# Performance work log

Measured on AMD Instinct MI355X. Metric: run time of the kernel, lower is better.

Reference implementation:

```python
import jax, jax.numpy as jnp
import numpy as np

B, S, D, H = 4, 2048, 1024, 16
HD = D // H
ROPE_THETA = 10000.0


def setup_inputs() -> dict:
    key = jax.random.key(0)
    ks = jax.random.split(key, 5)
    scale = 1.0 / np.sqrt(D)
    inp = {
        "x": jax.random.normal(ks[0], (B, S, D), dtype=jnp.float32),
        "Wq": jax.random.normal(ks[1], (D, D), dtype=jnp.float32) * scale,
        "bq": jnp.zeros((D,), jnp.float32),
        "Wk": jax.random.normal(ks[2], (D, D), dtype=jnp.float32) * scale,
        "bk": jnp.zeros((D,), jnp.float32),
        "Wv": jax.random.normal(ks[3], (D, D), dtype=jnp.float32) * scale,
        "bv": jnp.zeros((D,), jnp.float32),
        "Wo": jax.random.normal(ks[4], (D, D), dtype=jnp.float32) * scale,
        "bo": jnp.zeros((D,), jnp.float32),
        # causal mask: True means masked (j > i), matching masked_fill semantics
        "attn_mask": jnp.triu(jnp.ones((S, S), dtype=bool), k=1),
    }
    return inp


def _rope(x):
    # x: [B, H, S, HD]; half-split rotary embedding
    half = HD // 2
    inv_freq = 1.0 / (ROPE_THETA ** (jnp.arange(0, half, dtype=jnp.float32) / half))
    pos = jnp.arange(x.shape[2], dtype=jnp.float32)
    freqs = pos[:, None] * inv_freq[None, :]            # [S, half]
    cos = jnp.cos(freqs)[None, None]                    # [1,1,S,half]
    sin = jnp.sin(freqs)[None, None]
    x1, x2 = x[..., :half], x[..., half:]
    return jnp.concatenate([x1 * cos - x2 * sin, x2 * cos + x1 * sin], axis=-1)


def reference(x, Wq, bq, Wk, bk, Wv, bv, Wo, bo, attn_mask):
    def shape(t):  # [B,S,D] -> [B,H,S,HD]
        return t.reshape(B, S, H, HD).transpose(0, 2, 1, 3)

    q = shape(x @ Wq.T + bq)
    k = shape(x @ Wk.T + bk)
    v = shape(x @ Wv.T + bv)
    q = _rope(q)
    k = _rope(k)
    scores = jnp.einsum("bhqd,bhkd->bhqk", q, k) * (HD ** -0.5)
    scores = jnp.where(attn_mask[None, None], -jnp.inf, scores)
    w = jax.nn.softmax(scores, axis=-1)
    attn = jnp.einsum("bhqk,bhkd->bhqd", w, v)
    merged = attn.transpose(0, 2, 1, 3).reshape(B, S, D)
    return merged @ Wo.T + bo
```

## Files before the change

### kernel.cpp

```cpp
#include <hip/hip_runtime.h>
#include <math.h>

#define BATCH 4
#define SEQ   2048
#define DMODEL 1024
#define NHEAD 16
#define HDIM  64
#define MROWS (BATCH*SEQ)

typedef unsigned short u16;
typedef unsigned int   u32;

using bf16x8 = __attribute__((ext_vector_type(8))) short;
using f32x4  = __attribute__((ext_vector_type(4))) float;
using f32x16 = __attribute__((ext_vector_type(16))) float;
using u32x4  = __attribute__((ext_vector_type(4))) unsigned int;

__device__ __forceinline__ u16 f2bf(float f) {
    u32 u = __float_as_uint(f);
    u += 0x7fffu + ((u >> 16) & 1u);
    return (u16)(u >> 16);
}
__device__ __forceinline__ u32 pack2bf(float a, float b) {
    u32 ua = __float_as_uint(a); ua += 0x7fffu + ((ua >> 16) & 1u);
    u32 ub = __float_as_uint(b); ub += 0x7fffu + ((ub >> 16) & 1u);
    return (ua >> 16) | (ub & 0xffff0000u);
}
__device__ __forceinline__ u32 cvtpk(float a, float b) {
    u32 r;
    asm("v_cvt_pk_bf16_f32 %0, %1, %2" : "=v"(r) : "v"(a), "v"(b));
    return r;
}
#define PLSWAP(a, b) asm("v_permlane32_swap_b32 %0, %1" : "+v"(a), "+v"(b))

#define GLOBAL_LOAD_LDS16(gp, lp)                                              \
    __builtin_amdgcn_global_load_lds(                                          \
        (const __attribute__((address_space(1))) void*)(gp),                   \
        (__attribute__((address_space(3))) void*)(lp), 16, 0, 0)

__global__ __launch_bounds__(256) void convert_inputs(
    const float* __restrict__ x,  const float* __restrict__ wq,
    const float* __restrict__ wk, const float* __restrict__ wv,
    const float* __restrict__ wo, u16* __restrict__ dst)
{
    long long i4 = ((long long)blockIdx.x * 256 + threadIdx.x) * 4;
    const float* src; long long off;
    if (i4 < 8388608LL) { src = x; off = i4; }
    else {
        long long j = i4 - 8388608LL;
        int seg = (int)(j >> 20);
        off = j & 1048575LL;
        src = (seg == 0) ? wq : (seg == 1) ? wk : (seg == 2) ? wv : wo;
    }
    float4 v = *(const float4*)(src + off);
    u32 lo = (u32)f2bf(v.x) | ((u32)f2bf(v.y) << 16);
    u32 hi = (u32)f2bf(v.z) | ((u32)f2bf(v.w) << 16);
    *(uint2*)(dst + i4) = make_uint2(lo, hi);
}

template<int EPI>
__global__ __launch_bounds__(512) void gemm8(
    const u16* __restrict__ A, const u16* __restrict__ W,
    const float* __restrict__ b0_, const float* __restrict__ b1_,
    u16* __restrict__ C0_, u16* __restrict__ C1_, float* __restrict__ Cf)
{
    __shared__ __align__(16) u16 smem[65536];

    const int t    = threadIdx.x;
    const int lane = t & 63;
    const int w    = t >> 6;
    const int quad = lane >> 4;
    const int l15  = lane & 15;
    const int wm   = w >> 2;
    const int wn   = w & 3;

    const int bx  = blockIdx.x;
    const int xcd = bx & 7;
    const int i_  = bx >> 3;
    const int bml = i_ & 3;
    const int n_  = i_ >> 2;

    const int bm = (xcd * 4 + bml) * 256;
    const int bn = n_ * 256;

    const bool   isq  = (bn < 1024);
    const float* bias = isq ? b0_ : b1_;
    u16*         Cb   = isq ? C0_ : C1_;
    const int    bnl  = bn & 1023;

    const int sr8 = lane >> 3;
    const int scl = (lane & 7) ^ sr8;
    const u16* gA = A + (size_t)(bm + 8 * w + sr8) * DMODEL + scl * 8;
    const u16* gB = W + (size_t)(bn + 8 * w + sr8) * DMODEL + scl * 8;

#define STG_A(rg, kt, bs)                                                      \
    GLOBAL_LOAD_LDS16(gA + (size_t)(rg) * 64 * DMODEL + (kt) * 64,             \
                      &smem[(bs) * 16384 + ((rg) * 64 + 8 * w) * 64])
#define STG_B(rg, kt, bs)                                                      \
    GLOBAL_LOAD_LDS16(gB + (size_t)(rg) * 64 * DMODEL + (kt) * 64,             \
                      &smem[32768 + (bs) * 16384 + ((rg) * 64 + 8 * w) * 64])

    STG_B(0, 0, 0); STG_B(1, 0, 0); STG_B(2, 0, 0); STG_B(3, 0, 0);
    STG_A(0, 0, 0); STG_A(2, 0, 0); STG_A(1, 0, 0); STG_A(3, 0, 0);
    STG_B(0, 1, 1); STG_B(1, 1, 1); STG_B(2, 1, 1); STG_B(3, 1, 1);
    STG_A(0, 1, 1); STG_A(2, 1, 1);
    asm volatile("s_waitcnt vmcnt(6)" ::: "memory");
    __builtin_amdgcn_s_barrier();

    const int cA0 = (quad ^ (l15 & 7)) * 8;

    f32x4 acc[8][4] = {};
    bf16x8 bfr[4][2];

#define LOAD_B(Bb) {                                                           \
    _Pragma("unroll")                                                          \
    for (int j = 0; j < 4; ++j) {                                              \
        bfr[j][0] = *(const bf16x8*)&(Bb)[(wn * 64 + 16 * j + l15) * 64 + cA0];\
        bfr[j][1] = *(const bf16x8*)&(Bb)[(wn * 64 + 16 * j + l15) * 64 + (cA0 ^ 32)];\
    } }
#define PHASE(q, Ab, Bb, STAGES, CKPT) {                                       \
    bf16x8 af_[2][2];                                                          \
    if ((q) == 0) LOAD_B(Bb);                                                  \
    _Pragma("unroll")                                                          \
    for (int ii = 0; ii < 2; ++ii) {                                           \
        const int r_ = (wm * 128 + (q) * 32 + 16 * ii + l15) * 64;             \
        af_[ii][0] = *(const bf16x8*)&(Ab)[r_ + cA0];                          \
        af_[ii][1] = *(const bf16x8*)&(Ab)[r_ + (cA0 ^ 32)];                   \
    }                                                                          \
    STAGES;                                                                    \
    __builtin_amdgcn_s_barrier();                                              \
    asm volatile("s_waitcnt lgkmcnt(0)" ::: "memory");                         \
    __builtin_amdgcn_sched_barrier(0);                                         \
    __builtin_amdgcn_s_setprio(1);                                             \
    _Pragma("unroll")                                                          \
    for (int ii = 0; ii < 2; ++ii)                                             \
        _Pragma("unroll")                                                      \
        for (int j = 0; j < 4; ++j) {                                          \
            acc[2*(q)+ii][j] = __builtin_amdgcn_mfma_f32_16x16x32_bf16(        \
                af_[ii][0], bfr[j][0], acc[2*(q)+ii][j], 0, 0, 0);             \
            acc[2*(q)+ii][j] = __builtin_amdgcn_mfma_f32_16x16x32_bf16(        \
                af_[ii][1], bfr[j][1], acc[2*(q)+ii][j], 0, 0, 0);             \
        }                                                                      \
    __builtin_amdgcn_s_setprio(0);                                             \
    CKPT;                                                                      \
    __builtin_amdgcn_s_barrier();                                              \
}

    #pragma unroll 1
    for (int i = 0; i < 8; ++i) {
        const bool st = (i < 7);
        const int  kn = 2 * i + 2, kn3 = 2 * i + 3, ko = 2 * i + 1;
        {
            const u16* Ab = smem;
            const u16* Bb = smem + 32768;
            PHASE(0, Ab, Bb, { STG_A(1, ko, 1); STG_A(3, ko, 1); }, {});
            PHASE(1, Ab, Bb, { if (st) { STG_B(0, kn, 0); STG_B(1, kn, 0); } }, {});
            PHASE(2, Ab, Bb, { if (st) { STG_B(2, kn, 0); STG_B(3, kn, 0); } }, {});
            PHASE(3, Ab, Bb, { if (st) { STG_A(0, kn, 0); STG_A(2, kn, 0); } },
                  { if (st) asm volatile("s_waitcnt vmcnt(6)" ::: "memory");
                    else    asm volatile("s_waitcnt vmcnt(0)" ::: "memory"); });
        }
        {
            const u16* Ab = smem + 16384;
            const u16* Bb = smem + 32768 + 16384;
            PHASE(0, Ab, Bb, { if (st) { STG_A(1, kn, 0); STG_A(3, kn, 0); } }, {});
            PHASE(1, Ab, Bb, { if (st) { STG_B(0, kn3, 1); STG_B(1, kn3, 1); } }, {});
            PHASE(2, Ab, Bb, { if (st) { STG_B(2, kn3, 1); STG_B(3, kn3, 1); } }, {});
            PHASE(3, Ab, Bb, { if (st) { STG_A(0, kn3, 1); STG_A(2, kn3, 1); } },
                  { if (st) asm volatile("s_waitcnt vmcnt(6)" ::: "memory");
                    else    asm volatile("s_waitcnt vmcnt(0)" ::: "memory"); });
        }
    }
#undef PHASE
#undef LOAD_B
#undef STG_A
#undef STG_B

    const int wrow = wm * 128;
    const int wcol = wn * 64;
    float bvv[4];
    #pragma unroll
    for (int j = 0; j < 4; j++) bvv[j] = bias[bnl + wcol + 16 * j + l15];

    const float qscale = isq ? 0.18033688011112042f : 1.0f;
    float inv[2];
    #pragma unroll
    for (int j = 0; j < 2; j++) {
        int d = 16 * j + l15;
        inv[j] = exp2f(-(float)d * 0.4152410118609203f);
    }
    #pragma unroll
    for (int ri = 0; ri < 8; ri++)
        #pragma unroll
        for (int r = 0; r < 4; r++) {
            int mg = bm + wrow + 16 * ri + quad * 4 + r;
            int s  = mg & (SEQ - 1);
            #pragma unroll
            for (int j = 0; j < 2; j++) {
                float f = (float)s * inv[j];
                float sn, cs;
                __sincosf(f, &sn, &cs);
                float a1 = acc[ri][j][r]     + bvv[j];
                float a2 = acc[ri][j + 2][r] + bvv[j + 2];
                float o1 = (a1 * cs - a2 * sn) * qscale;
                float o2 = (a2 * cs + a1 * sn) * qscale;
                Cb[(size_t)mg * DMODEL + bnl + wcol + 16 * j       + l15] = f2bf(o1);
                Cb[(size_t)mg * DMODEL + bnl + wcol + 16 * (j + 2) + l15] = f2bf(o2);
            }
        }
}

template<int MODE>
__global__ __launch_bounds__(512) void gemm_bn128(
    const u16* __restrict__ A, const u16* __restrict__ W,
    const float* __restrict__ bias_, u16* __restrict__ Cb, float* __restrict__ Cf)
{
    __shared__ u16 As[3 * 256 * 64];
    __shared__ u16 Ws[3 * 128 * 64];

    const int t    = threadIdx.x;
    const int lane = t & 63;
    const int w    = t >> 6;
    const int quad = lane >> 4;
    const int l15  = lane & 15;

    const int bx  = blockIdx.x;
    const int xcd = bx & 7;
    const int i_  = bx >> 3;
    const int bml = i_ & 3;
    const int n_  = i_ >> 2;

    const int bm   = (xcd * 4 + bml) * 256;
    const int bn   = n_ * 128;
    const int wrow = (w >> 1) * 64;
    const int wcol = (w & 1) * 64;

    const int sr8 = lane >> 3;
    const int scl = (lane & 7) ^ sr8;
    const u16* gA = A + (size_t)(bm + 8 * w + sr8) * DMODEL + scl * 8;
    const u16* gB = W + (size_t)(bn + 8 * w + sr8) * DMODEL + scl * 8;

#define STAGE_A(li, kt, bs)                                                    \
    GLOBAL_LOAD_LDS16(gA + (size_t)(li) * 64 * DMODEL + (kt) * 64,             \
                      &As[(bs) * 16384 + ((li) * 64 + 8 * w) * 64])
#define STAGE_B(li, kt, bs)                                                    \
    GLOBAL_LOAD_LDS16(gB + (size_t)(li) * 64 * DMODEL + (kt) * 64,             \
                      &Ws[(bs) * 8192 + ((li) * 64 + 8 * w) * 64])

    STAGE_A(0, 0, 0); STAGE_A(1, 0, 0); STAGE_A(2, 0, 0); STAGE_A(3, 0, 0);
    STAGE_B(0, 0, 0); STAGE_B(1, 0, 0);
    STAGE_A(0, 1, 1); STAGE_A(1, 1, 1); STAGE_A(2, 1, 1); STAGE_A(3, 1, 1);
    STAGE_B(0, 1, 1); STAGE_B(1, 1, 1);
    asm volatile("s_waitcnt vmcnt(6)" ::: "memory");
    __builtin_amdgcn_s_barrier();

    const int c0 = (quad ^ (l15 & 7)) * 8;
    const int c1 = c0 ^ 32;

    f32x4 acc[4][4] = {};

    int bsel = 0;
    #pragma unroll 1
    for (int kt = 0; kt < DMODEL / 64; ++kt) {
        const u16* Ab = &As[bsel * 16384];
        const u16* Bb = &Ws[bsel * 8192];
        const int  ks = kt + 2;
        const int  sb = (bsel >= 1) ? bsel - 1 : 2;
        const bool st = (ks < DMODEL / 64);

        bf16x8 af[4], bfr[4];

        #pragma unroll
        for (int i = 0; i < 4; ++i)
            af[i] = *(const bf16x8*)&Ab[(wrow + 16 * i + l15) * 64 + c0];
        #pragma unroll
        for (int j = 0; j < 4; ++j)
            bfr[j] = *(const bf16x8*)&Bb[(wcol + 16 * j + l15) * 64 + c0];
        if (st) { STAGE_A(0, ks, sb); STAGE_A(1, ks, sb); STAGE_A(2, ks, sb); }
        __builtin_amdgcn_s_barrier();
        __builtin_amdgcn_s_setprio(1);
        #pragma unroll
        for (int i = 0; i < 4; ++i)
            #pragma unroll
            for (int j = 0; j < 4; ++j)
                acc[i][j] = __builtin_amdgcn_mfma_f32_16x16x32_bf16(af[i], bfr[j], acc[i][j], 0, 0, 0);
        __builtin_amdgcn_s_setprio(0);
        __builtin_amdgcn_s_barrier();

        #pragma unroll
        for (int i = 0; i < 4; ++i)
            af[i] = *(const bf16x8*)&Ab[(wrow + 16 * i + l15) * 64 + c1];
        #pragma unroll
        for (int j = 0; j < 4; ++j)
            bfr[j] = *(const bf16x8*)&Bb[(wcol + 16 * j + l15) * 64 + c1];
        if (st) { STAGE_A(3, ks, sb); STAGE_B(0, ks, sb); STAGE_B(1, ks, sb); }
        __builtin_amdgcn_s_barrier();
        __builtin_amdgcn_s_setprio(1);
        #pragma unroll
        for (int i = 0; i < 4; ++i)
            #pragma unroll
            for (int j = 0; j < 4; ++j)
                acc[i][j] = __builtin_amdgcn_mfma_f32_16x16x32_bf16(af[i], bfr[j], acc[i][j], 0, 0, 0);
        __builtin_amdgcn_s_setprio(0);
        if (st) asm volatile("s_waitcnt vmcnt(6)" ::: "memory");
        else    asm volatile("s_waitcnt vmcnt(0)" ::: "memory");
        __builtin_amdgcn_s_barrier();

        bsel = (bsel == 2) ? 0 : bsel + 1;
    }
#undef STAGE_A
#undef STAGE_B

    float bv[4];
    #pragma unroll
    for (int j = 0; j < 4; j++) bv[j] = bias_[bn + wcol + 16 * j + l15];

    if constexpr (MODE == 0) {
        #pragma unroll
        for (int i = 0; i < 4; i++)
            #pragma unroll
            for (int r = 0; r < 4; r++) {
                int mg = bm + wrow + 16 * i + quad * 4 + r;
                #pragma unroll
                for (int j = 0; j < 4; j++)
                    Cf[(size_t)mg * DMODEL + bn + wcol + 16 * j + l15] = acc[i][j][r] + bv[j];
            }
    } else {
        u16* T = As;
        #pragma unroll
        for (int i = 0; i < 4; i++) {
            #pragma unroll
            for (int j = 0; j < 4; j++) {
                int col = wrow + 16 * i + quad * 4;
                int row = wcol + 16 * j + l15;
                u32 lo = pack2bf(acc[i][j][0] + bv[j], acc[i][j][1] + bv[j]);
                u32 hi = pack2bf(acc[i][j][2] + bv[j], acc[i][j][3] + bv[j]);
                *(uint2*)((char*)T + row * 512 + ((col * 2) ^ ((row & 3) << 4)))
                    = make_uint2(lo, hi);
            }
        }
        __syncthreads();
        {
            int row  = t >> 2, colc = t & 3;
            int hgl  = (bn + row) >> 6;
            int dl   = (bn + row) & 63;
            int bb   = bm >> 11;
            size_t obase = (((size_t)(bb * NHEAD + hgl)) * HDIM + dl) * SEQ
                         + (bm & (SEQ - 1)) + colc * 64;
            #pragma unroll
            for (int k = 0; k < 8; k++) {
                uint4 vv = *(const uint4*)((const char*)T + row * 512
                             + ((colc * 128 + k * 16) ^ ((row & 3) << 4)));
                *(uint4*)(Cb + obase + k * 8) = vv;
            }
        }
    }
}

__global__ __launch_bounds__(256) void attn_mfma(
    const u16* __restrict__ Q, const u16* __restrict__ K,
    const u16* __restrict__ VT, u16* __restrict__ O)
{
    __shared__ __align__(16) u16 smem[16640];
    u16* const Qs  = smem;
    u16* const Ks0 = smem + 8192;
    u16* const Ks1 = smem;
    u16* const Vt0 = smem + 12288;
    u16* const Vt1 = smem + 4096;
    float* const lS = (float*)(smem + 16384);

    const int t    = threadIdx.x;
    const int lane = t & 63;
    const int w    = t >> 6;
    const int l31  = lane & 31;
    const int hl   = lane >> 5;
    const int bid  = blockIdx.x;
    const int bh   = bid & 63;
    const int x_   = bid >> 6, g_ = x_ >> 2, r_ = x_ & 3;
    const int qt   = (g_ == 0) ? 15 - r_ : (g_ == 1) ? 8 + r_
                   : (g_ == 2) ? 4 + r_ : 3 - r_;
    const int h    = bh & (NHEAD - 1);
    const int b    = bh >> 4;
    const int q0   = qt * 128;

    const size_t gbase = ((size_t)b * SEQ) * DMODEL + h * HDIM;
    const size_t vbase = ((size_t)(b * NHEAD + h)) * HDIM * SEQ;

    const int rl  = lane >> 3;
    const int csw = (lane & 7) ^ rl;

    #pragma unroll
    for (int i = 0; i < 4; i++) {
        int row = 32 * w + 8 * i + rl;
        GLOBAL_LOAD_LDS16(Q + gbase + (size_t)(q0 + row) * DMODEL + csw * 8,
                          &Qs[(32 * w + 8 * i) * 64]);
    }
    #pragma unroll
    for (int i = 0; i < 2; i++) {
        int row = 16 * w + 8 * i + rl;
        GLOBAL_LOAD_LDS16(K + gbase + (size_t)row * DMODEL + csw * 8,
                          &Ks0[(16 * w + 8 * i) * 64]);
        GLOBAL_LOAD_LDS16(VT + vbase + (size_t)row * SEQ + csw * 8,
                          &Vt0[(16 * w + 8 * i) * 64]);
    }
    __syncthreads();

    bf16x8 qf[4];
    {
        int row = 32 * w + l31;
        #pragma unroll
        for (int s = 0; s < 4; s++) {
            int c = (hl + 2 * s) ^ (row & 7);
            qf[s] = *(const bf16x8*)&Qs[row * 64 + c * 8];
        }
    }
    __syncthreads();

    float lsum = 0.0f;
    f32x16 oacc[2] = {};
    const int qg   = q0 + 32 * w + l31;
    const int qmax = q0 + 32 * w + 31;

#define QUADRANT(KRH, F0, F1) do {                                             \
    f32x16 s_ = {};                                                            \
    __builtin_amdgcn_s_setprio(1);                                             \
    _Pragma("unroll")                                                          \
    for (int stp_ = 0; stp_ < 4; ++stp_) {                                     \
        int c_ = ((hl + 2 * stp_) ^ (l31 & 7)) * 8;                            \
        bf16x8 ka_ = *(const bf16x8*)&Ksb[(32 * (KRH) + l31) * 64 + c_];       \
        s_ = __builtin_amdgcn_mfma_f32_32x32x16_bf16(ka_, qf[stp_], s_, 0, 0, 0);\
    }                                                                          \
    __builtin_amdgcn_s_setprio(0);                                             \
    if (k0 + 32 * (KRH) + 31 > q0 + 32 * w) {                                  \
        _Pragma("unroll")                                                      \
        for (int rr_ = 0; rr_ < 16; ++rr_) {                                   \
            int krg_ = k0 + 32 * (KRH) + (rr_ & 3) + 8 * (rr_ >> 2) + 4 * hl;  \
            if (krg_ > qg) s_[rr_] = -1e30f;                                   \
        }                                                                      \
    }                                                                          \
    float pv_[16];                                                             \
    _Pragma("unroll")                                                          \
    for (int rr_ = 0; rr_ < 16; ++rr_) pv_[rr_] = __builtin_amdgcn_exp2f(s_[rr_]);\
    lsum += ((pv_[0]+pv_[1])+(pv_[2]+pv_[3])) + ((pv_[4]+pv_[5])+(pv_[6]+pv_[7]))\
          + ((pv_[8]+pv_[9])+(pv_[10]+pv_[11])) + ((pv_[12]+pv_[13])+(pv_[14]+pv_[15]));\
    u32 k01_ = cvtpk(pv_[0], pv_[1]),   k23_ = cvtpk(pv_[2], pv_[3]);          \
    u32 k45_ = cvtpk(pv_[4], pv_[5]),   k67_ = cvtpk(pv_[6], pv_[7]);          \
    u32 k89_ = cvtpk(pv_[8], pv_[9]),   kab_ = cvtpk(pv_[10], pv_[11]);        \
    u32 kcd_ = cvtpk(pv_[12], pv_[13]), kef_ = cvtpk(pv_[14], pv_[15]);        \
    PLSWAP(k01_, k45_); PLSWAP(k23_, k67_);                                    \
    PLSWAP(k89_, kcd_); PLSWAP(kab_, kef_);                                    \
    { union { u32x4 u; bf16x8 v; } c0_; c0_.u = (u32x4){k01_, k23_, k45_, k67_};\
      F0 = c0_.v; }                                                            \
    { union { u32x4 u; bf16x8 v; } c1_; c1_.u = (u32x4){k89_, kab_, kcd_, kef_};\
      F1 = c1_.v; }                                                            \
} while (0)

#define PVSTEP(STP, PF) do {                                                   \
    int c_ = ((hl + 2 * (STP)) ^ (l31 & 7)) * 8;                               \
    bf16x8 v0_ = *(const bf16x8*)&Vtb[l31 * 64 + c_];                          \
    bf16x8 v1_ = *(const bf16x8*)&Vtb[(32 + l31) * 64 + c_];                   \
    oacc[0] = __builtin_amdgcn_mfma_f32_32x32x16_bf16(PF, v0_, oacc[0], 0, 0, 0);\
    oacc[1] = __builtin_amdgcn_mfma_f32_32x32x16_bf16(PF, v1_, oacc[1], 0, 0, 0);\
} while (0)

    const int ktn = 2 * qt + 2;
    for (int kt = 0; kt < ktn; kt++) {
        const int k0 = kt * 64;
        u16* const Ksb = (kt & 1) ? Ks1 : Ks0;
        u16* const Vtb = (kt & 1) ? Vt1 : Vt0;

        if (kt + 1 < ktn) {
            u16* const Ksn = (kt & 1) ? Ks0 : Ks1;
            u16* const Vtn = (kt & 1) ? Vt0 : Vt1;
            const size_t kk0 = (size_t)(kt + 1) * 64;
            #pragma unroll
            for (int i = 0; i < 2; i++) {
                int row = 16 * w + 8 * i + rl;
                GLOBAL_LOAD_LDS16(K + gbase + (kk0 + row) * DMODEL + csw * 8,
                                  &Ksn[(16 * w + 8 * i) * 64]);
                GLOBAL_LOAD_LDS16(VT + vbase + (size_t)row * SEQ + kk0 + csw * 8,
                                  &Vtn[(16 * w + 8 * i) * 64]);
            }
        }

        if (k0 <= qmax) {
            const bool q2 = (k0 + 32 <= qmax);
            bf16x8 pa0, pa1, pa2, pa3;
            QUADRANT(0, pa0, pa1);
            __builtin_amdgcn_s_setprio(1);
            PVSTEP(0, pa0); PVSTEP(1, pa1);
            __builtin_amdgcn_s_setprio(0);
            if (q2) {
                QUADRANT(1, pa2, pa3);
                __builtin_amdgcn_s_setprio(1);
                PVSTEP(2, pa2); PVSTEP(3, pa3);
                __builtin_amdgcn_s_setprio(0);
            }
        }
        asm volatile("s_waitcnt vmcnt(0)" ::: "memory");
        __builtin_amdgcn_s_barrier();
    }
#undef QUADRANT
#undef PVSTEP

    lsum += __shfl_xor(lsum, 32, 64);
    if (lane < 32) lS[32 * w + lane] = lsum;
    __syncthreads();

    #pragma unroll
    for (int g = 0; g < 4; g++) {
        f32x4 lv = *(const f32x4*)&lS[32 * w + 8 * g + 4 * hl];
        #pragma unroll
        for (int rr = 0; rr < 4; rr++) {
            int qg2 = q0 + 32 * w + rr + 8 * g + 4 * hl;
            float inv = 1.0f / lv[rr];
            #pragma unroll
            for (int dh = 0; dh < 2; dh++) {
                float o = oacc[dh][4 * g + rr] * inv;
                O[gbase + (size_t)qg2 * DMODEL + 32 * dh + l31] = f2bf(o);
            }
        }
    }
}

extern "C" void kernel_launch(void* const* d_in, const int* in_sizes, int n_in,
                              void* d_out, int out_size, void* d_ws, size_t ws_size,
                              hipStream_t stream)
{
    const float* x  = (const float*)d_in[0];
    const float* Wq = (const float*)d_in[1];
    const float* bq = (const float*)d_in[2];
    const float* Wk = (const float*)d_in[3];
    const float* bk = (const float*)d_in[4];
    const float* Wv = (const float*)d_in[5];
    const float* bv = (const float*)d_in[6];
    const float* Wo = (const float*)d_in[7];
    const float* bo = (const float*)d_in[8];

    u16* wsp = (u16*)d_ws;
    u16* xb  = wsp;
    u16* Wqb = wsp + 8388608;
    u16* Wkb = Wqb + 1048576;
    u16* Wvb = Wkb + 1048576;
    u16* Wob = Wvb + 1048576;
    u16* Qb  = Wob + 1048576;
    u16* Kb  = Qb + 8388608;
    u16* Vb  = Kb + 8388608;
    u16* Ab  = Vb + 8388608;

    convert_inputs<<<12288, 256, 0, stream>>>(x, Wq, Wk, Wv, Wo, xb);

    gemm8<0><<<256, 512, 0, stream>>>(xb, Wqb, bq, bk, Qb, Kb, nullptr);

    gemm_bn128<1><<<256, 512, 0, stream>>>(xb, Wvb, bv, Vb, nullptr);

    attn_mfma<<<1024, 256, 0, stream>>>(Qb, Kb, Vb, Ab);

    gemm_bn128<0><<<256, 512, 0, stream>>>(Ab, Wob, bo, nullptr, (float*)d_out);
}
```

Before: 256.1 us.

## Compute softmax row sums via MFMA with ones and change LDS swizzle

Replaces the per-thread VALU summation of exponentiated scores with an extra MFMA per PV step that multiplies the bf16 probabilities by a ones vector, so the row sums land in the same accumulator layout as the output. This removes the shuffle, the LDS staging of sums and a block barrier in the epilogue. It also changes the XOR swizzle of Q/K/V tiles in LDS to also depend on row>>3, aiming to cut bank conflicts. The cost is one extra MFMA per PV step (a third more PV matrix work), and the sums are now taken over bf16-rounded probabilities, which slightly changes numerics.

```diff
diff --git a/kernel.cpp b/kernel.cpp
--- a/kernel.cpp
+++ b/kernel.cpp
@@ -361,13 +361,12 @@
     const u16* __restrict__ Q, const u16* __restrict__ K,
     const u16* __restrict__ VT, u16* __restrict__ O)
 {
-    __shared__ __align__(16) u16 smem[16640];
+    __shared__ __align__(16) u16 smem[16384];
     u16* const Qs  = smem;
     u16* const Ks0 = smem + 8192;
     u16* const Ks1 = smem;
     u16* const Vt0 = smem + 12288;
     u16* const Vt1 = smem + 4096;
-    float* const lS = (float*)(smem + 16384);
 
     const int t    = threadIdx.x;
     const int lane = t & 63;
@@ -387,20 +386,22 @@
     const size_t vbase = ((size_t)(b * NHEAD + h)) * HDIM * SEQ;
 
     const int rl  = lane >> 3;
-    const int csw = (lane & 7) ^ rl;
+    const int cs0 = (lane & 7) ^ rl;
 
     #pragma unroll
     for (int i = 0; i < 4; i++) {
         int row = 32 * w + 8 * i + rl;
-        GLOBAL_LOAD_LDS16(Q + gbase + (size_t)(q0 + row) * DMODEL + csw * 8,
+        int c   = cs0 ^ i;
+        GLOBAL_LOAD_LDS16(Q + gbase + (size_t)(q0 + row) * DMODEL + c * 8,
                           &Qs[(32 * w + 8 * i) * 64]);
     }
     #pragma unroll
     for (int i = 0; i < 2; i++) {
         int row = 16 * w + 8 * i + rl;
-        GLOBAL_LOAD_LDS16(K + gbase + (size_t)row * DMODEL + csw * 8,
+        int c   = cs0 ^ ((2 * w + i) & 3);
+        GLOBAL_LOAD_LDS16(K + gbase + (size_t)row * DMODEL + c * 8,
                           &Ks0[(16 * w + 8 * i) * 64]);
-        GLOBAL_LOAD_LDS16(VT + vbase + (size_t)row * SEQ + csw * 8,
+        GLOBAL_LOAD_LDS16(VT + vbase + (size_t)row * SEQ + c * 8,
                           &Vt0[(16 * w + 8 * i) * 64]);
     }
     __syncthreads();
@@ -408,25 +409,31 @@
     bf16x8 qf[4];
     {
         int row = 32 * w + l31;
+        int rk  = (l31 & 7) ^ (l31 >> 3);
         #pragma unroll
         for (int s = 0; s < 4; s++) {
-            int c = (hl + 2 * s) ^ (row & 7);
+            int c = (hl + 2 * s) ^ rk;
             qf[s] = *(const bf16x8*)&Qs[row * 64 + c * 8];
         }
     }
     __syncthreads();
 
-    float lsum = 0.0f;
+    bf16x8 onesf;
+    #pragma unroll
+    for (int e = 0; e < 8; e++) onesf[e] = (short)0x3F80;
+
     f32x16 oacc[2] = {};
+    f32x16 lacc    = {};
     const int qg   = q0 + 32 * w + l31;
     const int qmax = q0 + 32 * w + 31;
+    const int rk31 = (l31 & 7) ^ (l31 >> 3);
 
 #define QUADRANT(KRH, F0, F1) do {                                             \
     f32x16 s_ = {};                                                            \
     __builtin_amdgcn_s_setprio(1);                                             \
     _Pragma("unroll")                                                          \
     for (int stp_ = 0; stp_ < 4; ++stp_) {                                     \
-        int c_ = ((hl + 2 * stp_) ^ (l31 & 7)) * 8;                            \
+        int c_ = ((hl + 2 * stp_) ^ rk31) * 8;                                 \
         bf16x8 ka_ = *(const bf16x8*)&Ksb[(32 * (KRH) + l31) * 64 + c_];       \
         s_ = __builtin_amdgcn_mfma_f32_32x32x16_bf16(ka_, qf[stp_], s_, 0, 0, 0);\
     }                                                                          \
@@ -441,8 +448,6 @@
     float pv_[16];                                                             \
     _Pragma("unroll")                                                          \
     for (int rr_ = 0; rr_ < 16; ++rr_) pv_[rr_] = __builtin_amdgcn_exp2f(s_[rr_]);\
-    lsum += ((pv_[0]+pv_[1])+(pv_[2]+pv_[3])) + ((pv_[4]+pv_[5])+(pv_[6]+pv_[7]))\
-          + ((pv_[8]+pv_[9])+(pv_[10]+pv_[11])) + ((pv_[12]+pv_[13])+(pv_[14]+pv_[15]));\
     u32 k01_ = cvtpk(pv_[0], pv_[1]),   k23_ = cvtpk(pv_[2], pv_[3]);          \
     u32 k45_ = cvtpk(pv_[4], pv_[5]),   k67_ = cvtpk(pv_[6], pv_[7]);          \
     u32 k89_ = cvtpk(pv_[8], pv_[9]),   kab_ = cvtpk(pv_[10], pv_[11]);        \
@@ -456,11 +461,12 @@
 } while (0)
 
 #define PVSTEP(STP, PF) do {                                                   \
-    int c_ = ((hl + 2 * (STP)) ^ (l31 & 7)) * 8;                               \
+    int c_ = ((hl + 2 * (STP)) ^ rk31) * 8;                                    \
     bf16x8 v0_ = *(const bf16x8*)&Vtb[l31 * 64 + c_];                          \
     bf16x8 v1_ = *(const bf16x8*)&Vtb[(32 + l31) * 64 + c_];                   \
     oacc[0] = __builtin_amdgcn_mfma_f32_32x32x16_bf16(PF, v0_, oacc[0], 0, 0, 0);\
     oacc[1] = __builtin_amdgcn_mfma_f32_32x32x16_bf16(PF, v1_, oacc[1], 0, 0, 0);\
+    lacc    = __builtin_amdgcn_mfma_f32_32x32x16_bf16(PF, onesf, lacc, 0, 0, 0);\
 } while (0)
 
     const int ktn = 2 * qt + 2;
@@ -476,9 +482,10 @@
             #pragma unroll
             for (int i = 0; i < 2; i++) {
                 int row = 16 * w + 8 * i + rl;
-                GLOBAL_LOAD_LDS16(K + gbase + (kk0 + row) * DMODEL + csw * 8,
+                int c   = cs0 ^ ((2 * w + i) & 3);
+                GLOBAL_LOAD_LDS16(K + gbase + (kk0 + row) * DMODEL + c * 8,
                                   &Ksn[(16 * w + 8 * i) * 64]);
-                GLOBAL_LOAD_LDS16(VT + vbase + (size_t)row * SEQ + kk0 + csw * 8,
+                GLOBAL_LOAD_LDS16(VT + vbase + (size_t)row * SEQ + kk0 + c * 8,
                                   &Vtn[(16 * w + 8 * i) * 64]);
             }
         }
@@ -503,17 +510,12 @@
 #undef QUADRANT
 #undef PVSTEP
 
-    lsum += __shfl_xor(lsum, 32, 64);
-    if (lane < 32) lS[32 * w + lane] = lsum;
-    __syncthreads();
-
     #pragma unroll
     for (int g = 0; g < 4; g++) {
-        f32x4 lv = *(const f32x4*)&lS[32 * w + 8 * g + 4 * hl];
         #pragma unroll
         for (int rr = 0; rr < 4; rr++) {
             int qg2 = q0 + 32 * w + rr + 8 * g + 4 * hl;
-            float inv = 1.0f / lv[rr];
+            float inv = 1.0f / lacc[4 * g + rr];
             #pragma unroll
             for (int dh = 0; dh < 2; dh++) {
                 float o = oacc[dh][4 * g + rr] * inv;
```

After: 259.3 us (median of 2 runs). Within noise of the previous version (+1.3%).
